# Performance work log

Measured on AMD Instinct MI355X. Metric: run time of the kernel, lower is better.

The kernel has to match this reference:

```python
import jax, jax.numpy as jnp
import numpy as np

B, T = 2, 512
D, H, DFF = 1024, 16, 4096
V, CSL = 32000, 16
NL, NDL = 4, 2
MAXLEN = 1024
DH = D // H


def generate_ar_mask(L, csl):
    m = np.zeros((2 * L, 2 * L), dtype=bool)
    for i in range(L):
        m[:i] = True
        m[L + (i // csl) * csl: L + i] = True
    return jnp.asarray(m)


def generate_block_ntp_mask(L, csl):
    m = np.zeros((2 * L, 2 * L), dtype=bool)
    for c in range(L // csl):
        if c - 1 >= 0:
            m[:(c - 1) * csl] = True
        m[L + c * csl: L + (c + 1) * csl] = True
    return jnp.asarray(m)


def layernorm(x, g, b, eps=1e-5):
    mu = x.mean(-1, keepdims=True)
    var = x.var(-1, keepdims=True)
    return (x - mu) / jnp.sqrt(var + eps) * g + b


def block(x, mask, p):
    ln1g, ln1b, wqkv, bqkv, wo, bo, ln2g, ln2b, w1, b1, w2, b2 = p
    h = layernorm(x, ln1g, ln1b)
    qkv = h @ wqkv + bqkv                       # [B,S,3D]
    q, k, v = jnp.split(qkv, 3, axis=-1)
    bs, S, _ = x.shape
    q = q.reshape(bs, S, H, DH).transpose(0, 2, 1, 3)
    k = k.reshape(bs, S, H, DH).transpose(0, 2, 1, 3)
    v = v.reshape(bs, S, H, DH).transpose(0, 2, 1, 3)
    scores = jnp.einsum('bhqd,bhkd->bhqk', q, k) / jnp.sqrt(jnp.asarray(DH, x.dtype))
    scores = jnp.where(mask, scores, jnp.asarray(-1e9, x.dtype))
    attn = jax.nn.softmax(scores, axis=-1)
    o = jnp.einsum('bhqk,bhkd->bhqd', attn, v)
    o = o.transpose(0, 2, 1, 3).reshape(bs, S, D)
    x = x + (o @ wo + bo)
    h = layernorm(x, ln2g, ln2b)
    return x + (jax.nn.gelu(h @ w1 + b1, approximate=False) @ w2 + b2)


def setup_inputs():
    key = jax.random.key(0)
    ks = jax.random.split(key, 6)

    def pstack(k, n):
        kk = jax.random.split(k, 4)
        return dict(
            ln1g=jnp.ones((n, D)), ln1b=jnp.zeros((n, D)),
            wqkv=0.02 * jax.random.normal(kk[0], (n, D, 3 * D)), bqkv=jnp.zeros((n, 3 * D)),
            wo=0.02 * jax.random.normal(kk[1], (n, D, D)), bo=jnp.zeros((n, D)),
            ln2g=jnp.ones((n, D)), ln2b=jnp.zeros((n, D)),
            w1=0.02 * jax.random.normal(kk[2], (n, D, DFF)), b1=jnp.zeros((n, DFF)),
            w2=0.02 * jax.random.normal(kk[3], (n, DFF, D)), b2=jnp.zeros((n, D)))

    body = pstack(ks[0], NL)
    dec = pstack(ks[1], NDL)
    inp = {
        'tok_ids': jax.random.randint(ks[2], (B, T), 0, V),
        'tok_emb': 0.02 * jax.random.normal(ks[3], (V, D)),
        'pos_emb': 0.02 * jax.random.normal(ks[4], (MAXLEN, D)),
        'mask_tokens': 0.02 * jax.random.normal(ks[5], (1, CSL, D)),
    }
    for kname, vv in body.items():
        inp['b_' + kname] = vv
    for kname, vv in dec.items():
        inp['d_' + kname] = vv
    return inp


def reference(tok_ids, tok_emb, pos_emb, mask_tokens,
              b_ln1g, b_ln1b, b_wqkv, b_bqkv, b_wo, b_bo, b_ln2g, b_ln2b, b_w1, b_b1, b_w2, b_b2,
              d_ln1g, d_ln1b, d_wqkv, d_bqkv, d_wo, d_bo, d_ln2g, d_ln2b, d_w1, d_b1, d_w2, d_b2):
    Bq, Tq = tok_ids.shape
    pos = jnp.tile(jnp.arange(Tq), 2)            # pos ids repeated for both halves
    emb_pos = pos_emb[pos]                       # [2T, D], broadcast over batch
    mask_ids = jnp.tile(mask_tokens, (Bq, Tq // CSL, 1))
    x = jnp.concatenate([tok_emb[tok_ids], mask_ids], axis=1) + emb_pos[None]

    body_mask = generate_block_ntp_mask(Tq, CSL)
    bp = (b_ln1g, b_ln1b, b_wqkv, b_bqkv, b_wo, b_bo, b_ln2g, b_ln2b, b_w1, b_b1, b_w2, b_b2)
    for i in range(NL):
        x = block(x, body_mask, tuple(p[i] for p in bp))

    ar_mask = generate_ar_mask(Tq, CSL)
    dp = (d_ln1g, d_ln1b, d_wqkv, d_bqkv, d_wo, d_bo, d_ln2g, d_ln2b, d_w1, d_b1, d_w2, d_b2)
    for i in range(NDL):
        x = block(x, ar_mask, tuple(p[i] for p in dp))

    logits = (x @ tok_emb.T)[:, Tq + 1:, :]      # [B, T-1, V]
    tgt = tok_ids[:, :-1].reshape(-1)
    logits = logits.reshape(-1, V)
    logp = jax.nn.log_softmax(logits, axis=-1)
    loss = -jnp.take_along_axis(logp, tgt[:, None], axis=1).mean()
    return loss
```

## Files before the change

kernel.cpp:

```cpp
#include <hip/hip_runtime.h>
#include <hip/hip_bf16.h>
#include <math.h>

#define DD   1024
#define HHN  16
#define DHD  64
#define DFFN 4096
#define VV   32000
#define BBN  2
#define TTN  512
#define SSN  1024
#define NRN  2048

typedef __attribute__((ext_vector_type(8))) short short8;
typedef __attribute__((ext_vector_type(4))) float f32x4;

enum : long {
    LSTR    = 12582912,
    OFF_QKV = 0,
    OFF_WO  = 3145728,
    OFF_W1  = 4194304,
    OFF_W2  = 8388608
};

struct P24 { const float* p[24]; };

__device__ __forceinline__ unsigned short f2bf(float f) {
    __hip_bfloat16 h = __float2bfloat16(f);
    return __builtin_bit_cast(unsigned short, h);
}
__device__ __forceinline__ float bf2f(unsigned short u) {
    return __bfloat162float(__builtin_bit_cast(__hip_bfloat16, u));
}

__device__ __forceinline__ void glds16(const void* g, void* l) {
    __builtin_amdgcn_global_load_lds(
        (const __attribute__((address_space(1))) void*)g,
        (__attribute__((address_space(3))) void*)l,
        16, 0, 0);
}

__device__ __forceinline__ float blockReduceSum(float v) {
    __shared__ float sh[4];
    #pragma unroll
    for (int o = 1; o < 64; o <<= 1) v += __shfl_xor(v, o, 64);
    int lane = threadIdx.x & 63, wv = threadIdx.x >> 6;
    __syncthreads();
    if (lane == 0) sh[wv] = v;
    __syncthreads();
    return sh[0] + sh[1] + sh[2] + sh[3];
}

__global__ __launch_bounds__(256) void prep_k(P24 wp, unsigned short* __restrict__ wbf,
                                              const int* __restrict__ tok,
                                              const float* __restrict__ temb,
                                              const float* __restrict__ pemb,
                                              const float* __restrict__ mtok,
                                              float* __restrict__ x) {
    __shared__ __align__(16) unsigned short Lb[256][72];
    const int id = blockIdx.x;
    const int t = threadIdx.x;

    if (id < 4608) {
        int seg, base, K, N;
        long woff;
        if (id < 1152)      { seg = 0; base = 0;    K = DD;   N = 3 * DD; woff = OFF_QKV; }
        else if (id < 1536) { seg = 1; base = 1152; K = DD;   N = DD;     woff = OFF_WO;  }
        else if (id < 3072) { seg = 2; base = 1536; K = DD;   N = DFFN;   woff = OFF_W1;  }
        else                { seg = 3; base = 3072; K = DFFN; N = DD;     woff = OFF_W2;  }
        const int rid = id - base;
        const int tpl = (K / 256) * (N / 64);
        const int lz = rid / tpl, t2 = rid % tpl;
        const int nt = N / 64;
        const int n0 = (t2 % nt) * 64, k0 = (t2 / nt) * 256;
        const float* w = wp.p[seg * 6 + lz];
        unsigned short* wt = wbf + (size_t)lz * LSTR + woff;

        #pragma unroll
        for (int p = 0; p < 2; p++) {
            const int k = p * 128 + (t >> 1);
            const int nch = (t & 1) * 32;
            const float* src = w + (size_t)(k0 + k) * N + n0 + nch;
            __align__(16) unsigned short tmp[32];
            #pragma unroll
            for (int i = 0; i < 8; i++) {
                float4 f = ((const float4*)src)[i];
                tmp[i * 4 + 0] = f2bf(f.x); tmp[i * 4 + 1] = f2bf(f.y);
                tmp[i * 4 + 2] = f2bf(f.z); tmp[i * 4 + 3] = f2bf(f.w);
            }
            #pragma unroll
            for (int i = 0; i < 4; i++)
                *(int4*)&Lb[k][nch + i * 8] = *(const int4*)&tmp[i * 8];
        }
        __syncthreads();
        {
            const int row = t >> 2, kc = (t & 3) * 64;
            __align__(16) unsigned short tmp[64];
            #pragma unroll
            for (int i = 0; i < 64; i++) tmp[i] = Lb[kc + i][row];
            unsigned short* dst = wt + (size_t)(n0 + row) * K + k0 + kc;
            #pragma unroll
            for (int i = 0; i < 8; i++)
                *(int4*)(dst + i * 8) = *(const int4*)&tmp[i * 8];
        }
    } else {
        const int row = id - 4608;
        const int b = row >> 10, s = row & 1023;
        const int d = t * 4;
        const float* src;
        const float* pe;
        if (s < TTN) {
            int tid2 = tok[b * TTN + s];
            src = temb + (size_t)tid2 * DD + d;
            pe  = pemb + (size_t)s * DD + d;
        } else {
            int sm = s - TTN;
            src = mtok + (size_t)(sm & 15) * DD + d;
            pe  = pemb + (size_t)sm * DD + d;
        }
        float4 v = *(const float4*)src;
        float4 p = *(const float4*)pe;
        v.x += p.x; v.y += p.y; v.z += p.z; v.w += p.w;
        *(float4*)(x + (size_t)row * DD + d) = v;
    }
}

__global__ __launch_bounds__(256) void ln_k(const float* __restrict__ x,
                                            const float* __restrict__ g,
                                            const float* __restrict__ b,
                                            unsigned short* __restrict__ out) {
    int row = blockIdx.x;
    int d = threadIdx.x * 4;
    const float4 v = *(const float4*)(x + (size_t)row * DD + d);
    float s  = v.x + v.y + v.z + v.w;
    float ss = v.x * v.x + v.y * v.y + v.z * v.z + v.w * v.w;
    s  = blockReduceSum(s);
    ss = blockReduceSum(ss);
    float mu  = s * (1.0f / DD);
    float var = ss * (1.0f / DD) - mu * mu;
    float inv = rsqrtf(var + 1e-5f);
    const float4 gg = *(const float4*)(g + d);
    const float4 bb = *(const float4*)(b + d);
    ushort4 o;
    o.x = f2bf((v.x - mu) * inv * gg.x + bb.x);
    o.y = f2bf((v.y - mu) * inv * gg.y + bb.y);
    o.z = f2bf((v.z - mu) * inv * gg.z + bb.z);
    o.w = f2bf((v.w - mu) * inv * gg.w + bb.w);
    *(ushort4*)(out + (size_t)row * DD + d) = o;
}

__global__ __launch_bounds__(256, 2) void flash_k(
    const unsigned short* __restrict__ qkvb,
    unsigned short* __restrict__ o,
    int mtype) {
    __shared__ __align__(16) unsigned short Qs[128][72];
    __shared__ __align__(16) unsigned short Ks[64][72];
    __shared__ __align__(16) unsigned short Vs[64][72];
    __shared__ __align__(16) unsigned short Ps[128][72];
    __shared__ float vcol[64];

    const int blk = blockIdx.x;
    const int bh = blk >> 3, qt = blk & 7;
    const int b = bh >> 4, h = bh & 15;
    const int t = threadIdx.x;
    const int lane = t & 63;
    const int w = t >> 6;
    const int fr = lane & 15;
    const int g8 = (lane >> 4) * 8;
    const int g4 = (lane >> 4) * 4;

    {
        const int r = t >> 1, c0 = (t & 1) * 32;
        const unsigned short* src =
            qkvb + (size_t)(b * SSN + qt * 128 + r) * 3072 + h * 64 + c0;
        *(int4*)&Qs[r][c0]      = *(const int4*)(src);
        *(int4*)&Qs[r][c0 + 8]  = *(const int4*)(src + 8);
        *(int4*)&Qs[r][c0 + 16] = *(const int4*)(src + 16);
        *(int4*)&Qs[r][c0 + 24] = *(const int4*)(src + 24);
    }
    __syncthreads();
    short8 aq[2][2];
    #pragma unroll
    for (int m = 0; m < 2; m++)
        #pragma unroll
        for (int kk = 0; kk < 2; kk++)
            aq[m][kk] = *(const short8*)&Qs[w * 32 + m * 16 + fr][kk * 32 + g8];

    float mrun[2][4], lrun[2][4];
    f32x4 accO[2][4] = {};
    #pragma unroll
    for (int m = 0; m < 2; m++)
        #pragma unroll
        for (int j = 0; j < 4; j++) { mrun[m][j] = -1e30f; lrun[m][j] = 0.f; }

    float vacc[16];
    #pragma unroll
    for (int j = 0; j < 16; j++) vacc[j] = 0.f;

    const unsigned short* kbase = qkvb + (size_t)(b * SSN) * 3072 + DD + h * 64;
    const unsigned short* vbase = qkvb + (size_t)(b * SSN) * 3072 + 2 * DD + h * 64;
    const int d0 = w * 16;

    for (int kt = 0; kt < 16; kt++) {
        __syncthreads();
        {
            const int r = t >> 2, c0 = (t & 3) * 16;
            const unsigned short* src = kbase + (size_t)(kt * 64 + r) * 3072 + c0;
            *(int4*)&Ks[r][c0]     = *(const int4*)(src);
            *(int4*)&Ks[r][c0 + 8] = *(const int4*)(src + 8);
        }
        {
            const unsigned short* src = vbase + (size_t)(kt * 64 + lane) * 3072 + d0;
            int4 q0 = *(const int4*)(src);
            int4 q1 = *(const int4*)(src + 8);
            const unsigned short* u = (const unsigned short*)&q0;
            #pragma unroll
            for (int j = 0; j < 8; j++) {
                Vs[d0 + j][lane] = u[j];
                vacc[j] += bf2f(u[j]);
            }
            const unsigned short* u2 = (const unsigned short*)&q1;
            #pragma unroll
            for (int j = 0; j < 8; j++) {
                Vs[d0 + 8 + j][lane] = u2[j];
                vacc[8 + j] += bf2f(u2[j]);
            }
        }
        __syncthreads();

        short8 bk[4][2];
        #pragma unroll
        for (int n = 0; n < 4; n++)
            #pragma unroll
            for (int kk = 0; kk < 2; kk++)
                bk[n][kk] = *(const short8*)&Ks[n * 16 + fr][kk * 32 + g8];

        #pragma unroll
        for (int m = 0; m < 2; m++) {
            f32x4 a2[4] = {};
            #pragma unroll
            for (int n = 0; n < 4; n++) {
                a2[n] = __builtin_amdgcn_mfma_f32_16x16x32_bf16(aq[m][0], bk[n][0], a2[n], 0, 0, 0);
                a2[n] = __builtin_amdgcn_mfma_f32_16x16x32_bf16(aq[m][1], bk[n][1], a2[n], 0, 0, 0);
            }
            #pragma unroll
            for (int j = 0; j < 4; j++) {
                float tm = fmaxf(fmaxf(a2[0][j], a2[1][j]), fmaxf(a2[2][j], a2[3][j]));
                tm *= 0.125f;
                #pragma unroll
                for (int o2 = 1; o2 < 16; o2 <<= 1) tm = fmaxf(tm, __shfl_xor(tm, o2, 64));
                const float mn = fmaxf(mrun[m][j], tm);
                const float alpha = __expf(mrun[m][j] - mn);
                mrun[m][j] = mn;
                float rs = 0.f;
                #pragma unroll
                for (int n = 0; n < 4; n++) {
                    float pv = __expf(a2[n][j] * 0.125f - mn);
                    rs += pv;
                    Ps[w * 32 + m * 16 + g4 + j][n * 16 + fr] = f2bf(pv);
                }
                #pragma unroll
                for (int o2 = 1; o2 < 16; o2 <<= 1) rs += __shfl_xor(rs, o2, 64);
                lrun[m][j] = lrun[m][j] * alpha + rs;
                #pragma unroll
                for (int nd = 0; nd < 4; nd++) accO[m][nd][j] *= alpha;
            }
        }
        #pragma unroll
        for (int kk = 0; kk < 2; kk++) {
            short8 pa0 = *(const short8*)&Ps[w * 32 + fr][kk * 32 + g8];
            short8 pa1 = *(const short8*)&Ps[w * 32 + 16 + fr][kk * 32 + g8];
            #pragma unroll
            for (int nd = 0; nd < 4; nd++) {
                short8 vb = *(const short8*)&Vs[nd * 16 + fr][kk * 32 + g8];
                accO[0][nd] = __builtin_amdgcn_mfma_f32_16x16x32_bf16(pa0, vb, accO[0][nd], 0, 0, 0);
                accO[1][nd] = __builtin_amdgcn_mfma_f32_16x16x32_bf16(pa1, vb, accO[1][nd], 0, 0, 0);
            }
        }
    }

    #pragma unroll
    for (int j = 0; j < 16; j++) {
        float vs = vacc[j];
        #pragma unroll
        for (int o2 = 1; o2 < 64; o2 <<= 1) vs += __shfl_xor(vs, o2, 64);
        if (lane == j) vcol[d0 + j] = vs;
    }
    __syncthreads();

    #pragma unroll
    for (int m = 0; m < 2; m++)
        #pragma unroll
        for (int nd = 0; nd < 4; nd++)
            #pragma unroll
            for (int j = 0; j < 4; j++) {
                const int row = qt * 128 + w * 32 + m * 16 + g4 + j;
                const int col = nd * 16 + fr;
                bool uni;
                if (mtype == 0) uni = (row >= 480 && row < 512);
                else            uni = (row == 511) || (row >= 512 && (row & 15) == 15);
                float val;
                if (uni) val = vcol[col] * (1.0f / 1024.0f);
                else     val = accO[m][nd][j] / lrun[m][j];
                o[(size_t)(b * SSN + row) * DD + h * 64 + col] = f2bf(val);
            }
}

template <bool DOLN>
__global__ __launch_bounds__(256) void rln_k(const float* __restrict__ pp,
                                             const float* __restrict__ bias,
                                             float* __restrict__ x,
                                             const float* __restrict__ g,
                                             const float* __restrict__ b,
                                             unsigned short* __restrict__ xb,
                                             unsigned short* __restrict__ xl) {
    const int row = blockIdx.x;
    const int d = threadIdx.x * 4;
    const size_t off = (size_t)row * DD + d;
    float4 v = *(const float4*)(x + off);
    #pragma unroll
    for (int sl = 0; sl < 4; sl++) {
        float4 p = *(const float4*)(pp + (size_t)sl * NRN * DD + off);
        v.x += p.x; v.y += p.y; v.z += p.z; v.w += p.w;
    }
    const float4 bv = *(const float4*)(bias + d);
    v.x += bv.x; v.y += bv.y; v.z += bv.z; v.w += bv.w;
    *(float4*)(x + off) = v;
    if (DOLN) {
        float s  = v.x + v.y + v.z + v.w;
        float ss = v.x * v.x + v.y * v.y + v.z * v.z + v.w * v.w;
        s  = blockReduceSum(s);
        ss = blockReduceSum(ss);
        float mu  = s * (1.0f / DD);
        float var = ss * (1.0f / DD) - mu * mu;
        float inv = rsqrtf(var + 1e-5f);
        const float4 gg = *(const float4*)(g + d);
        const float4 bb = *(const float4*)(b + d);
        ushort4 ov;
        ov.x = f2bf((v.x - mu) * inv * gg.x + bb.x);
        ov.y = f2bf((v.y - mu) * inv * gg.y + bb.y);
        ov.z = f2bf((v.z - mu) * inv * gg.z + bb.z);
        ov.w = f2bf((v.w - mu) * inv * gg.w + bb.w);
        *(ushort4*)(xb + off) = ov;
    } else {
        const int s = row & 1023;
        if (s >= 513) {
            const int xr = (row >> 10) * 511 + (s - 513);
            ushort4 ov;
            ov.x = f2bf(v.x); ov.y = f2bf(v.y); ov.z = f2bf(v.z); ov.w = f2bf(v.w);
            *(ushort4*)(xl + (size_t)xr * DD + d) = ov;
        }
    }
}

__global__ __launch_bounds__(256) void loss_row2_k(const float2* __restrict__ part,
                                                   const float* __restrict__ tgtlog,
                                                   float* __restrict__ rowloss) {
    const int r = blockIdx.x;
    const int t = threadIdx.x;
    float mx = -1e30f, s = 0.f;
    for (int i = t; i < 500; i += 256) {
        float2 p = part[(size_t)r * 500 + i];
        float m2 = fmaxf(mx, p.x);
        s = s * __expf(mx - m2) + p.y * __expf(p.x - m2);
        mx = m2;
    }
    #pragma unroll
    for (int o2 = 1; o2 < 64; o2 <<= 1) {
        float om = __shfl_xor(mx, o2, 64);
        float os = __shfl_xor(s, o2, 64);
        float m2 = fmaxf(mx, om);
        s = s * __expf(mx - m2) + os * __expf(om - m2);
        mx = m2;
    }
    __shared__ float shm[4], shs[4];
    int lane = t & 63, wv = t >> 6;
    if (lane == 0) { shm[wv] = mx; shs[wv] = s; }
    __syncthreads();
    if (t == 0) {
        float M = fmaxf(fmaxf(shm[0], shm[1]), fmaxf(shm[2], shm[3]));
        float S = shs[0] * __expf(shm[0] - M) + shs[1] * __expf(shm[1] - M)
                + shs[2] * __expf(shm[2] - M) + shs[3] * __expf(shm[3] - M);
        rowloss[r] = (logf(S) + M) - tgtlog[r];
    }
}

__global__ __launch_bounds__(256) void loss_final_k(const float* __restrict__ rowloss,
                                                    float* __restrict__ out) {
    int t = threadIdx.x;
    float s = 0.f;
    for (int i = t; i < 1022; i += 256) s += rowloss[i];
    s = blockReduceSum(s);
    if (t == 0) out[0] = s * (1.0f / 1022.0f);
}

template <int EPI, int KSPLIT>
__global__ __launch_bounds__(256) void gemm_k(
    const unsigned short* __restrict__ A, long lda,
    const unsigned short* __restrict__ Bt, long ldb,
    void* __restrict__ Cp, long ldc,
    const float* __restrict__ bias,
    int MT, int K, long kstr) {
    __shared__ __align__(16) unsigned short As[2][128][32];
    __shared__ __align__(16) unsigned short Bs[2][128][32];

    const int nwg = gridDim.x;
    const int q = nwg >> 3, r = nwg & 7;
    const int xcd = blockIdx.x & 7, lin = blockIdx.x >> 3;
    const int wg = (xcd < r ? xcd * (q + 1) : r * (q + 1) + (xcd - r) * q) + lin;
    const int tiles = nwg / KSPLIT;
    const int ks = wg / tiles;
    const int rem = wg % tiles;
    const int brow = (rem % MT) * 128;
    const int bcol = (rem / MT) * 128;
    const int Kl = K / KSPLIT;

    const int t = threadIdx.x;
    const int lane = t & 63;
    const int w = t >> 6;
    const int fr = lane & 15;
    const int g8 = (lane >> 4) * 8;

    const int sr = w * 32 + (lane >> 2);
    const int sc = (lane & 3) * 8;
    const unsigned short* aP0 = A + (size_t)(brow + sr) * lda + ks * Kl + sc;
    const unsigned short* aP1 = aP0 + (size_t)16 * lda;
    const unsigned short* bP0 = Bt + (size_t)(bcol + sr) * ldb + ks * Kl + sc;
    const unsigned short* bP1 = bP0 + (size_t)16 * ldb;

    f32x4 acc[4][4] = {};
    const int nsteps = Kl >> 5;

    glds16(aP0, &As[0][w * 32][0]);
    glds16(aP1, &As[0][w * 32 + 16][0]);
    glds16(bP0, &Bs[0][w * 32][0]);
    glds16(bP1, &Bs[0][w * 32 + 16][0]);
    aP0 += 32; aP1 += 32; bP0 += 32; bP1 += 32;
    asm volatile("s_waitcnt vmcnt(0)");
    __syncthreads();

    int cur = 0;
    for (int s2 = 1; s2 < nsteps; ++s2) {
        const int nb = cur ^ 1;
        glds16(aP0, &As[nb][w * 32][0]);
        glds16(aP1, &As[nb][w * 32 + 16][0]);
        glds16(bP0, &Bs[nb][w * 32][0]);
        glds16(bP1, &Bs[nb][w * 32 + 16][0]);
        aP0 += 32; aP1 += 32; bP0 += 32; bP1 += 32;

        short8 af[4], bf[4];
        #pragma unroll
        for (int m = 0; m < 4; m++)
            af[m] = *(const short8*)&As[cur][(w >> 1) * 64 + m * 16 + fr][g8];
        #pragma unroll
        for (int n = 0; n < 4; n++)
            bf[n] = *(const short8*)&Bs[cur][(w & 1) * 64 + n * 16 + fr][g8];
        #pragma unroll
        for (int m = 0; m < 4; m++)
            #pragma unroll
            for (int n = 0; n < 4; n++)
                acc[m][n] = __builtin_amdgcn_mfma_f32_16x16x32_bf16(af[m], bf[n], acc[m][n], 0, 0, 0);
        __syncthreads();
        cur = nb;
    }
    {
        short8 af[4], bf[4];
        #pragma unroll
        for (int m = 0; m < 4; m++)
            af[m] = *(const short8*)&As[cur][(w >> 1) * 64 + m * 16 + fr][g8];
        #pragma unroll
        for (int n = 0; n < 4; n++)
            bf[n] = *(const short8*)&Bs[cur][(w & 1) * 64 + n * 16 + fr][g8];
        #pragma unroll
        for (int m = 0; m < 4; m++)
            #pragma unroll
            for (int n = 0; n < 4; n++)
                acc[m][n] = __builtin_amdgcn_mfma_f32_16x16x32_bf16(af[m], bf[n], acc[m][n], 0, 0, 0);
    }

    const int wr = (w >> 1) * 64;
    const int wc = (w & 1) * 64;
    const int g4 = (lane >> 4) * 4;
    #pragma unroll
    for (int n = 0; n < 4; n++) {
        const int col = bcol + wc + n * 16 + fr;
        const float bv = bias ? bias[col] : 0.f;
        #pragma unroll
        for (int m = 0; m < 4; m++) {
            #pragma unroll
            for (int j = 0; j < 4; j++) {
                const int row = brow + wr + m * 16 + g4 + j;
                float v = acc[m][n][j] + bv;
                const size_t ci = (size_t)row * ldc + col;
                if (EPI == 0) {
                    ((float*)Cp)[ci] = v;
                } else if (EPI == 1) {
                    ((unsigned short*)Cp)[ci] = f2bf(v);
                } else if (EPI == 2) {
                    float gl = 0.5f * v * (1.0f + erff(v * 0.70710678118654752f));
                    ((unsigned short*)Cp)[ci] = f2bf(gl);
                } else if (EPI == 3) {
                    ((float*)Cp)[ci] += v;
                } else {
                    ((float*)Cp)[(size_t)ks * kstr + ci] = v;
                }
            }
        }
    }
}

__global__ __launch_bounds__(256) void gemm_lse_k(
    const unsigned short* __restrict__ A,
    const float* __restrict__ Btf,
    float2* __restrict__ part,
    float* __restrict__ tgtlog,
    const int* __restrict__ tok) {
    __shared__ __align__(16) unsigned short As[2][128][32];
    __shared__ __align__(16) unsigned short Bs[2][128][40];

    const int nwg = gridDim.x;
    const int q = nwg >> 3, r = nwg & 7;
    const int xcd = blockIdx.x & 7, lin = blockIdx.x >> 3;
    const int wg = (xcd < r ? xcd * (q + 1) : r * (q + 1) + (xcd - r) * q) + lin;
    const int MT = 8;
    const int brow = (wg % MT) * 128;
    const int bcol = (wg / MT) * 128;

    const int t = threadIdx.x;
    const int lane = t & 63;
    const int w = t >> 6;
    const int fr = lane & 15;
    const int g8 = (lane >> 4) * 8;

    const int sra = w * 32 + (lane >> 2);
    const int sca = (lane & 3) * 8;
    const unsigned short* aP0 = A + (size_t)(brow + sra) * DD + sca;
    const unsigned short* aP1 = aP0 + (size_t)16 * DD;
    const int rb = w * 32 + (lane >> 1);
    const int kb = (lane & 1) * 16;
    const float* bP = Btf + (size_t)(bcol + rb) * DD + kb;

    f32x4 acc[4][4] = {};

    glds16(aP0, &As[0][w * 32][0]);
    glds16(aP1, &As[0][w * 32 + 16][0]);
    aP0 += 32; aP1 += 32;
    {
        __align__(16) unsigned short tmp[16];
        #pragma unroll
        for (int i = 0; i < 4; i++) {
            float4 f = ((const float4*)bP)[i];
            tmp[i * 4 + 0] = f2bf(f.x); tmp[i * 4 + 1] = f2bf(f.y);
            tmp[i * 4 + 2] = f2bf(f.z); tmp[i * 4 + 3] = f2bf(f.w);
        }
        *(int4*)&Bs[0][rb][kb]     = *(const int4*)&tmp[0];
        *(int4*)&Bs[0][rb][kb + 8] = *(const int4*)&tmp[8];
    }
    bP += 32;
    asm volatile("s_waitcnt vmcnt(0)");
    __syncthreads();

    int cur = 0;
    for (int s2 = 1; s2 < 32; ++s2) {
        const int nb = cur ^ 1;
        float4 f0 = ((const float4*)bP)[0];
        float4 f1 = ((const float4*)bP)[1];
        float4 f2 = ((const float4*)bP)[2];
        float4 f3 = ((const float4*)bP)[3];
        bP += 32;
        glds16(aP0, &As[nb][w * 32][0]);
        glds16(aP1, &As[nb][w * 32 + 16][0]);
        aP0 += 32; aP1 += 32;

        short8 af[4], bf[4];
        #pragma unroll
        for (int m = 0; m < 4; m++)
            af[m] = *(const short8*)&As[cur][(w >> 1) * 64 + m * 16 + fr][g8];
        #pragma unroll
        for (int n = 0; n < 4; n++)
            bf[n] = *(const short8*)&Bs[cur][(w & 1) * 64 + n * 16 + fr][g8];
        #pragma unroll
        for (int m = 0; m < 4; m++)
            #pragma unroll
            for (int n = 0; n < 4; n++)
                acc[m][n] = __builtin_amdgcn_mfma_f32_16x16x32_bf16(af[m], bf[n], acc[m][n], 0, 0, 0);

        {
            __align__(16) unsigned short tmp[16];
            tmp[0] = f2bf(f0.x); tmp[1] = f2bf(f0.y); tmp[2]  = f2bf(f0.z); tmp[3]  = f2bf(f0.w);
            tmp[4] = f2bf(f1.x); tmp[5] = f2bf(f1.y); tmp[6]  = f2bf(f1.z); tmp[7]  = f2bf(f1.w);
            tmp[8] = f2bf(f2.x); tmp[9] = f2bf(f2.y); tmp[10] = f2bf(f2.z); tmp[11] = f2bf(f2.w);
            tmp[12] = f2bf(f3.x); tmp[13] = f2bf(f3.y); tmp[14] = f2bf(f3.z); tmp[15] = f2bf(f3.w);
            *(int4*)&Bs[nb][rb][kb]     = *(const int4*)&tmp[0];
            *(int4*)&Bs[nb][rb][kb + 8] = *(const int4*)&tmp[8];
        }
        __syncthreads();
        cur = nb;
    }
    {
        short8 af[4], bf[4];
        #pragma unroll
        for (int m = 0; m < 4; m++)
            af[m] = *(const short8*)&As[cur][(w >> 1) * 64 + m * 16 + fr][g8];
        #pragma unroll
        for (int n = 0; n < 4; n++)
            bf[n] = *(const short8*)&Bs[cur][(w & 1) * 64 + n * 16 + fr][g8];
        #pragma unroll
        for (int m = 0; m < 4; m++)
            #pragma unroll
            for (int n = 0; n < 4; n++)
                acc[m][n] = __builtin_amdgcn_mfma_f32_16x16x32_bf16(af[m], bf[n], acc[m][n], 0, 0, 0);
    }

    const int wr = (w >> 1) * 64;
    const int wc = (w & 1) * 64;
    const int g4 = (lane >> 4) * 4;
    const int ct2 = (bcol >> 7) * 2 + (w & 1);
    #pragma unroll
    for (int m = 0; m < 4; m++) {
        #pragma unroll
        for (int j = 0; j < 4; j++) {
            const int grow = brow + wr + m * 16 + g4 + j;
            const float v0 = acc[m][0][j], v1 = acc[m][1][j];
            const float v2 = acc[m][2][j], v3 = acc[m][3][j];
            float mx = fmaxf(fmaxf(v0, v1), fmaxf(v2, v3));
            #pragma unroll
            for (int o2 = 1; o2 < 16; o2 <<= 1) mx = fmaxf(mx, __shfl_xor(mx, o2, 64));
            float s = __expf(v0 - mx) + __expf(v1 - mx) + __expf(v2 - mx) + __expf(v3 - mx);
            #pragma unroll
            for (int o2 = 1; o2 < 16; o2 <<= 1) s += __shfl_xor(s, o2, 64);
            if (fr == 0) {
                float2 p; p.x = mx; p.y = s;
                part[(size_t)grow * 500 + ct2] = p;
            }
            int tgtc = -1;
            if (grow < 511) tgtc = tok[grow];
            else if (grow >= 511 && grow < 1022) tgtc = tok[512 + grow - 511];
            const int cl = tgtc - (bcol + wc);
            if (tgtc >= 0 && cl >= 0 && cl < 64 && (cl & 15) == fr) {
                const float vv[4] = {v0, v1, v2, v3};
                tgtlog[grow] = vv[cl >> 4];
            }
        }
    }
}

extern "C" void kernel_launch(void* const* d_in, const int* in_sizes, int n_in,
                              void* d_out, int out_size, void* d_ws, size_t ws_size,
                              hipStream_t stream) {
    const int*   tok  = (const int*)d_in[0];
    const float* temb = (const float*)d_in[1];
    const float* pemb = (const float*)d_in[2];
    const float* mtok = (const float*)d_in[3];
    const float* W[24];
    for (int i = 0; i < 24; i++) W[i] = (const float*)d_in[4 + i];

    char* ws = (char*)d_ws;
    float*          x      = (float*)(ws + 0);
    unsigned short* xb     = (unsigned short*)(ws + 8388608);
    unsigned short* qkvb   = (unsigned short*)(ws + 12582912);
    unsigned short* o      = (unsigned short*)(ws + 25165824);
    unsigned short* g      = (unsigned short*)(ws + 29360128);
    float*          pp     = (float*)(ws + 46137344);
    unsigned short* wbf    = (unsigned short*)(ws + 79691776);
    float2*         part   = (float2*)(ws + 145227776);
    float*          tgtlog = (float*)(ws + 149327872);
    unsigned short* xl     = (unsigned short*)(ws + 230686720);
    float*          rowloss= (float*)(ws + 232783872);

    P24 wp;
    for (int l = 0; l < 6; l++) {
        const int grp = (l < 4) ? 0 : 1;
        const int li  = (l < 4) ? l : l - 4;
        const float* const* P = W + grp * 12;
        wp.p[0 + l]  = P[2]  + (size_t)li * DD * 3 * DD;
        wp.p[6 + l]  = P[4]  + (size_t)li * DD * DD;
        wp.p[12 + l] = P[8]  + (size_t)li * DD * DFFN;
        wp.p[18 + l] = P[10] + (size_t)li * DFFN * DD;
    }
    prep_k<<<4608 + 2048, 256, 0, stream>>>(wp, wbf, tok, temb, pemb, mtok, x);

    for (int l = 0; l < 6; l++) {
        const int grp = (l < 4) ? 0 : 1;
        const int li  = (l < 4) ? l : l - 4;
        const float* const* P = W + grp * 12;
        const float* ln1g = P[0] + (size_t)li * DD;
        const float* ln1b = P[1] + (size_t)li * DD;
        const float* bqkv = P[3] + (size_t)li * 3 * DD;
        const float* bo   = P[5] + (size_t)li * DD;
        const float* ln2g = P[6] + (size_t)li * DD;
        const float* ln2b = P[7] + (size_t)li * DD;
        const float* b1   = P[9] + (size_t)li * DFFN;
        const float* b2   = P[11] + (size_t)li * DD;
        unsigned short* wl = wbf + (size_t)l * LSTR;

        if (l == 0) ln_k<<<NRN, 256, 0, stream>>>(x, ln1g, ln1b, xb);
        gemm_k<1, 1><<<16 * 24, 256, 0, stream>>>(xb, DD, wl + OFF_QKV, DD,
                                                  qkvb, 3 * DD, bqkv, 16, DD, 0);
        flash_k<<<256, 256, 0, stream>>>(qkvb, o, grp);
        gemm_k<3, 1><<<16 * 8, 256, 0, stream>>>(o, DD, wl + OFF_WO, DD,
                                                 x, DD, bo, 16, DD, 0);

        ln_k<<<NRN, 256, 0, stream>>>(x, ln2g, ln2b, xb);
        gemm_k<2, 1><<<16 * 32, 256, 0, stream>>>(xb, DD, wl + OFF_W1, DD,
                                                  g, DFFN, b1, 16, DD, 0);
        gemm_k<4, 4><<<16 * 8 * 4, 256, 0, stream>>>(g, DFFN, wl + OFF_W2, DFFN,
                                                     pp, DD, nullptr, 16, DFFN,
                                                     (long)NRN * DD);
        if (l < 5) {
            const int l2 = l + 1;
            const int grp2 = (l2 < 4) ? 0 : 1;
            const int li2  = (l2 < 4) ? l2 : l2 - 4;
            const float* const* P2 = W + grp2 * 12;
            rln_k<true><<<NRN, 256, 0, stream>>>(pp, b2, x,
                                                 P2[0] + (size_t)li2 * DD,
                                                 P2[1] + (size_t)li2 * DD, xb, nullptr);
        } else {
            rln_k<false><<<NRN, 256, 0, stream>>>(pp, b2, x, nullptr, nullptr, nullptr, xl);
        }
    }

    gemm_lse_k<<<2000, 256, 0, stream>>>(xl, temb, part, tgtlog, tok);
    loss_row2_k<<<1022, 256, 0, stream>>>(part, tgtlog, rowloss);
    loss_final_k<<<1, 256, 0, stream>>>(rowloss, (float*)d_out);
}
```

Baseline: 1.578 ms.

## Halve flash attention query tile and pre-convert embedding to bf16 for LSE GEMM

The flash attention kernel now handles 64 query rows per block instead of 128, doubling the grid to 512 blocks with higher occupancy bounds and fewer registers per wave. The final logits GEMM no longer converts fp32 embedding rows to bf16 inside its main loop. A separate conversion kernel writes a bf16 copy of the embedding into the weight workspace, and the GEMM then loads it asynchronously straight into LDS. The trade-offs are that K/V tiles are reloaded twice as often across blocks, and the extra conversion pass adds a full read and write of the embedding table.

New measurement: 1.554 ms. About the same (-1.5%).

```diff
diff --git a/kernel.cpp b/kernel.cpp
--- a/kernel.cpp
+++ b/kernel.cpp
@@ -149,18 +149,30 @@
     *(ushort4*)(out + (size_t)row * DD + d) = o;
 }
 
-__global__ __launch_bounds__(256, 2) void flash_k(
+__global__ __launch_bounds__(256) void conv_k(const float* __restrict__ w,
+                                              unsigned short* __restrict__ o, long n) {
+    long i = ((long)blockIdx.x * 256 + threadIdx.x) * 8;
+    if (i >= n) return;
+    float4 a = *(const float4*)(w + i);
+    float4 b = *(const float4*)(w + i + 4);
+    __align__(16) unsigned short tmp[8];
+    tmp[0] = f2bf(a.x); tmp[1] = f2bf(a.y); tmp[2] = f2bf(a.z); tmp[3] = f2bf(a.w);
+    tmp[4] = f2bf(b.x); tmp[5] = f2bf(b.y); tmp[6] = f2bf(b.z); tmp[7] = f2bf(b.w);
+    *(int4*)(o + i) = *(const int4*)tmp;
+}
+
+__global__ __launch_bounds__(256, 4) void flash_k(
     const unsigned short* __restrict__ qkvb,
     unsigned short* __restrict__ o,
     int mtype) {
-    __shared__ __align__(16) unsigned short Qs[128][72];
+    __shared__ __align__(16) unsigned short Qs[64][72];
     __shared__ __align__(16) unsigned short Ks[64][72];
     __shared__ __align__(16) unsigned short Vs[64][72];
-    __shared__ __align__(16) unsigned short Ps[128][72];
+    __shared__ __align__(16) unsigned short Ps[64][72];
     __shared__ float vcol[64];
 
     const int blk = blockIdx.x;
-    const int bh = blk >> 3, qt = blk & 7;
+    const int bh = blk >> 4, qt = blk & 15;
     const int b = bh >> 4, h = bh & 15;
     const int t = threadIdx.x;
     const int lane = t & 63;
@@ -170,28 +182,22 @@
     const int g4 = (lane >> 4) * 4;
 
     {
-        const int r = t >> 1, c0 = (t & 1) * 32;
+        const int r = t >> 2, c0 = (t & 3) * 16;
         const unsigned short* src =
-            qkvb + (size_t)(b * SSN + qt * 128 + r) * 3072 + h * 64 + c0;
-        *(int4*)&Qs[r][c0]      = *(const int4*)(src);
-        *(int4*)&Qs[r][c0 + 8]  = *(const int4*)(src + 8);
-        *(int4*)&Qs[r][c0 + 16] = *(const int4*)(src + 16);
-        *(int4*)&Qs[r][c0 + 24] = *(const int4*)(src + 24);
+            qkvb + (size_t)(b * SSN + qt * 64 + r) * 3072 + h * 64 + c0;
+        *(int4*)&Qs[r][c0]     = *(const int4*)(src);
+        *(int4*)&Qs[r][c0 + 8] = *(const int4*)(src + 8);
     }
     __syncthreads();
-    short8 aq[2][2];
-    #pragma unroll
-    for (int m = 0; m < 2; m++)
-        #pragma unroll
-        for (int kk = 0; kk < 2; kk++)
-            aq[m][kk] = *(const short8*)&Qs[w * 32 + m * 16 + fr][kk * 32 + g8];
-
-    float mrun[2][4], lrun[2][4];
-    f32x4 accO[2][4] = {};
-    #pragma unroll
-    for (int m = 0; m < 2; m++)
-        #pragma unroll
-        for (int j = 0; j < 4; j++) { mrun[m][j] = -1e30f; lrun[m][j] = 0.f; }
+    short8 aq[2];
+    #pragma unroll
+    for (int kk = 0; kk < 2; kk++)
+        aq[kk] = *(const short8*)&Qs[w * 16 + fr][kk * 32 + g8];
+
+    float mrun[4], lrun[4];
+    f32x4 accO[4] = {};
+    #pragma unroll
+    for (int j = 0; j < 4; j++) { mrun[j] = -1e30f; lrun[j] = 0.f; }
 
     float vacc[16];
     #pragma unroll
@@ -228,53 +234,43 @@
         }
         __syncthreads();
 
-        short8 bk[4][2];
-        #pragma unroll
-        for (int n = 0; n < 4; n++)
-            #pragma unroll
-            for (int kk = 0; kk < 2; kk++)
-                bk[n][kk] = *(const short8*)&Ks[n * 16 + fr][kk * 32 + g8];
-
-        #pragma unroll
-        for (int m = 0; m < 2; m++) {
-            f32x4 a2[4] = {};
+        f32x4 a2[4] = {};
+        #pragma unroll
+        for (int n = 0; n < 4; n++) {
+            short8 bk0 = *(const short8*)&Ks[n * 16 + fr][g8];
+            short8 bk1 = *(const short8*)&Ks[n * 16 + fr][32 + g8];
+            a2[n] = __builtin_amdgcn_mfma_f32_16x16x32_bf16(aq[0], bk0, a2[n], 0, 0, 0);
+            a2[n] = __builtin_amdgcn_mfma_f32_16x16x32_bf16(aq[1], bk1, a2[n], 0, 0, 0);
+        }
+        #pragma unroll
+        for (int j = 0; j < 4; j++) {
+            float tm = fmaxf(fmaxf(a2[0][j], a2[1][j]), fmaxf(a2[2][j], a2[3][j]));
+            tm *= 0.125f;
+            #pragma unroll
+            for (int o2 = 1; o2 < 16; o2 <<= 1) tm = fmaxf(tm, __shfl_xor(tm, o2, 64));
+            const float mn = fmaxf(mrun[j], tm);
+            const float alpha = __expf(mrun[j] - mn);
+            mrun[j] = mn;
+            float rs = 0.f;
             #pragma unroll
             for (int n = 0; n < 4; n++) {
-                a2[n] = __builtin_amdgcn_mfma_f32_16x16x32_bf16(aq[m][0], bk[n][0], a2[n], 0, 0, 0);
-                a2[n] = __builtin_amdgcn_mfma_f32_16x16x32_bf16(aq[m][1], bk[n][1], a2[n], 0, 0, 0);
-            }
-            #pragma unroll
-            for (int j = 0; j < 4; j++) {
-                float tm = fmaxf(fmaxf(a2[0][j], a2[1][j]), fmaxf(a2[2][j], a2[3][j]));
-                tm *= 0.125f;
-                #pragma unroll
-                for (int o2 = 1; o2 < 16; o2 <<= 1) tm = fmaxf(tm, __shfl_xor(tm, o2, 64));
-                const float mn = fmaxf(mrun[m][j], tm);
-                const float alpha = __expf(mrun[m][j] - mn);
-                mrun[m][j] = mn;
-                float rs = 0.f;
-                #pragma unroll
-                for (int n = 0; n < 4; n++) {
-                    float pv = __expf(a2[n][j] * 0.125f - mn);
-                    rs += pv;
-                    Ps[w * 32 + m * 16 + g4 + j][n * 16 + fr] = f2bf(pv);
-                }
-                #pragma unroll
-                for (int o2 = 1; o2 < 16; o2 <<= 1) rs += __shfl_xor(rs, o2, 64);
-                lrun[m][j] = lrun[m][j] * alpha + rs;
-                #pragma unroll
-                for (int nd = 0; nd < 4; nd++) accO[m][nd][j] *= alpha;
-            }
+                float pv = __expf(a2[n][j] * 0.125f - mn);
+                rs += pv;
+                Ps[w * 16 + g4 + j][n * 16 + fr] = f2bf(pv);
+            }
+            #pragma unroll
+            for (int o2 = 1; o2 < 16; o2 <<= 1) rs += __shfl_xor(rs, o2, 64);
+            lrun[j] = lrun[j] * alpha + rs;
+            #pragma unroll
+            for (int nd = 0; nd < 4; nd++) accO[nd][j] *= alpha;
         }
         #pragma unroll
         for (int kk = 0; kk < 2; kk++) {
-            short8 pa0 = *(const short8*)&Ps[w * 32 + fr][kk * 32 + g8];
-            short8 pa1 = *(const short8*)&Ps[w * 32 + 16 + fr][kk * 32 + g8];
+            short8 pa = *(const short8*)&Ps[w * 16 + fr][kk * 32 + g8];
             #pragma unroll
             for (int nd = 0; nd < 4; nd++) {
                 short8 vb = *(const short8*)&Vs[nd * 16 + fr][kk * 32 + g8];
-                accO[0][nd] = __builtin_amdgcn_mfma_f32_16x16x32_bf16(pa0, vb, accO[0][nd], 0, 0, 0);
-                accO[1][nd] = __builtin_amdgcn_mfma_f32_16x16x32_bf16(pa1, vb, accO[1][nd], 0, 0, 0);
+                accO[nd] = __builtin_amdgcn_mfma_f32_16x16x32_bf16(pa, vb, accO[nd], 0, 0, 0);
             }
         }
     }
@@ -289,21 +285,19 @@
     __syncthreads();
 
     #pragma unroll
-    for (int m = 0; m < 2; m++)
-        #pragma unroll
-        for (int nd = 0; nd < 4; nd++)
-            #pragma unroll
-            for (int j = 0; j < 4; j++) {
-                const int row = qt * 128 + w * 32 + m * 16 + g4 + j;
-                const int col = nd * 16 + fr;
-                bool uni;
-                if (mtype == 0) uni = (row >= 480 && row < 512);
-                else            uni = (row == 511) || (row >= 512 && (row & 15) == 15);
-                float val;
-                if (uni) val = vcol[col] * (1.0f / 1024.0f);
-                else     val = accO[m][nd][j] / lrun[m][j];
-                o[(size_t)(b * SSN + row) * DD + h * 64 + col] = f2bf(val);
-            }
+    for (int nd = 0; nd < 4; nd++)
+        #pragma unroll
+        for (int j = 0; j < 4; j++) {
+            const int row = qt * 64 + w * 16 + g4 + j;
+            const int col = nd * 16 + fr;
+            bool uni;
+            if (mtype == 0) uni = (row >= 480 && row < 512);
+            else            uni = (row == 511) || (row >= 512 && (row & 15) == 15);
+            float val;
+            if (uni) val = vcol[col] * (1.0f / 1024.0f);
+            else     val = accO[nd][j] / lrun[j];
+            o[(size_t)(b * SSN + row) * DD + h * 64 + col] = f2bf(val);
+        }
 }
 
 template <bool DOLN>
@@ -511,12 +505,12 @@
 
 __global__ __launch_bounds__(256) void gemm_lse_k(
     const unsigned short* __restrict__ A,
-    const float* __restrict__ Btf,
+    const unsigned short* __restrict__ Bt,
     float2* __restrict__ part,
     float* __restrict__ tgtlog,
     const int* __restrict__ tok) {
     __shared__ __align__(16) unsigned short As[2][128][32];
-    __shared__ __align__(16) unsigned short Bs[2][128][40];
+    __shared__ __align__(16) unsigned short Bs[2][128][32];
 
     const int nwg = gridDim.x;
     const int q = nwg >> 3, r = nwg & 7;
@@ -532,45 +526,31 @@
     const int fr = lane & 15;
     const int g8 = (lane >> 4) * 8;
 
-    const int sra = w * 32 + (lane >> 2);
-    const int sca = (lane & 3) * 8;
-    const unsigned short* aP0 = A + (size_t)(brow + sra) * DD + sca;
+    const int sr = w * 32 + (lane >> 2);
+    const int sc = (lane & 3) * 8;
+    const unsigned short* aP0 = A + (size_t)(brow + sr) * DD + sc;
     const unsigned short* aP1 = aP0 + (size_t)16 * DD;
-    const int rb = w * 32 + (lane >> 1);
-    const int kb = (lane & 1) * 16;
-    const float* bP = Btf + (size_t)(bcol + rb) * DD + kb;
+    const unsigned short* bP0 = Bt + (size_t)(bcol + sr) * DD + sc;
+    const unsigned short* bP1 = bP0 + (size_t)16 * DD;
 
     f32x4 acc[4][4] = {};
 
     glds16(aP0, &As[0][w * 32][0]);
     glds16(aP1, &As[0][w * 32 + 16][0]);
-    aP0 += 32; aP1 += 32;
-    {
-        __align__(16) unsigned short tmp[16];
-        #pragma unroll
-        for (int i = 0; i < 4; i++) {
-            float4 f = ((const float4*)bP)[i];
-            tmp[i * 4 + 0] = f2bf(f.x); tmp[i * 4 + 1] = f2bf(f.y);
-            tmp[i * 4 + 2] = f2bf(f.z); tmp[i * 4 + 3] = f2bf(f.w);
-        }
-        *(int4*)&Bs[0][rb][kb]     = *(const int4*)&tmp[0];
-        *(int4*)&Bs[0][rb][kb + 8] = *(const int4*)&tmp[8];
-    }
-    bP += 32;
+    glds16(bP0, &Bs[0][w * 32][0]);
+    glds16(bP1, &Bs[0][w * 32 + 16][0]);
+    aP0 += 32; aP1 += 32; bP0 += 32; bP1 += 32;
     asm volatile("s_waitcnt vmcnt(0)");
     __syncthreads();
 
     int cur = 0;
     for (int s2 = 1; s2 < 32; ++s2) {
         const int nb = cur ^ 1;
-        float4 f0 = ((const float4*)bP)[0];
-        float4 f1 = ((const float4*)bP)[1];
-        float4 f2 = ((const float4*)bP)[2];
-        float4 f3 = ((const float4*)bP)[3];
-        bP += 32;
         glds16(aP0, &As[nb][w * 32][0]);
         glds16(aP1, &As[nb][w * 32 + 16][0]);
-        aP0 += 32; aP1 += 32;
+        glds16(bP0, &Bs[nb][w * 32][0]);
+        glds16(bP1, &Bs[nb][w * 32 + 16][0]);
+        aP0 += 32; aP1 += 32; bP0 += 32; bP1 += 32;
 
         short8 af[4], bf[4];
         #pragma unroll
@@ -584,16 +564,6 @@
             #pragma unroll
             for (int n = 0; n < 4; n++)
                 acc[m][n] = __builtin_amdgcn_mfma_f32_16x16x32_bf16(af[m], bf[n], acc[m][n], 0, 0, 0);
-
-        {
-            __align__(16) unsigned short tmp[16];
-            tmp[0] = f2bf(f0.x); tmp[1] = f2bf(f0.y); tmp[2]  = f2bf(f0.z); tmp[3]  = f2bf(f0.w);
-            tmp[4] = f2bf(f1.x); tmp[5] = f2bf(f1.y); tmp[6]  = f2bf(f1.z); tmp[7]  = f2bf(f1.w);
-            tmp[8] = f2bf(f2.x); tmp[9] = f2bf(f2.y); tmp[10] = f2bf(f2.z); tmp[11] = f2bf(f2.w);
-            tmp[12] = f2bf(f3.x); tmp[13] = f2bf(f3.y); tmp[14] = f2bf(f3.z); tmp[15] = f2bf(f3.w);
-            *(int4*)&Bs[nb][rb][kb]     = *(const int4*)&tmp[0];
-            *(int4*)&Bs[nb][rb][kb + 8] = *(const int4*)&tmp[8];
-        }
         __syncthreads();
         cur = nb;
     }
@@ -663,6 +633,7 @@
     unsigned short* g      = (unsigned short*)(ws + 29360128);
     float*          pp     = (float*)(ws + 46137344);
     unsigned short* wbf    = (unsigned short*)(ws + 79691776);
+    unsigned short* tembb  = (unsigned short*)(ws + 79691776);
     float2*         part   = (float2*)(ws + 145227776);
     float*          tgtlog = (float*)(ws + 149327872);
     unsigned short* xl     = (unsigned short*)(ws + 230686720);
@@ -697,7 +668,7 @@
         if (l == 0) ln_k<<<NRN, 256, 0, stream>>>(x, ln1g, ln1b, xb);
         gemm_k<1, 1><<<16 * 24, 256, 0, stream>>>(xb, DD, wl + OFF_QKV, DD,
                                                   qkvb, 3 * DD, bqkv, 16, DD, 0);
-        flash_k<<<256, 256, 0, stream>>>(qkvb, o, grp);
+        flash_k<<<512, 256, 0, stream>>>(qkvb, o, grp);
         gemm_k<3, 1><<<16 * 8, 256, 0, stream>>>(o, DD, wl + OFF_WO, DD,
                                                  x, DD, bo, 16, DD, 0);
 
@@ -720,7 +691,8 @@
         }
     }
 
-    gemm_lse_k<<<2000, 256, 0, stream>>>(xl, temb, part, tgtlog, tok);
+    conv_k<<<16000, 256, 0, stream>>>(temb, tembb, (long)VV * DD);
+    gemm_lse_k<<<2000, 256, 0, stream>>>(xl, tembb, part, tgtlog, tok);
     loss_row2_k<<<1022, 256, 0, stream>>>(part, tgtlog, rowloss);
     loss_final_k<<<1, 256, 0, stream>>>(rowloss, (float*)d_out);
 }
```
